# Kernel optimization log

Measured on AMD Instinct MI355X. Metric: run time of the kernel, lower is better.

Reference implementation:

```python
import jax, jax.numpy as jnp
import numpy as np

B, S, HID = 1, 2048, 4096
NH, NKV, HD = 32, 8, 128
WINDOW = 1024
ROPE_THETA = 1e6
NEG = -1e9


def rotate_half(x):
    x1, x2 = jnp.split(x, 2, axis=-1)
    return jnp.concatenate((-x2, x1), axis=-1)


def setup_inputs() -> dict:
    key = jax.random.key(0)
    ks = jax.random.split(key, 10)
    hidden_states = jax.random.normal(ks[0], (B, S, HID), jnp.float32)
    # rotary tables [max_pos, head_dim]
    inv_freq = 1.0 / (ROPE_THETA ** (jnp.arange(0, HD, 2, dtype=jnp.float32) / HD))
    t = jnp.arange(S, dtype=jnp.float32)
    freqs = jnp.outer(t, inv_freq)                       # [S, HD/2]
    emb = jnp.concatenate((freqs, freqs), axis=-1)       # [S, HD]
    cos, sin = jnp.cos(emb), jnp.sin(emb)
    position_ids = jnp.arange(S, dtype=jnp.int64)[None, :].astype(jnp.int32)
    # sliding-window causal additive mask [B,1,S,S]
    i = jnp.arange(S)[:, None]
    j = jnp.arange(S)[None, :]
    allowed = (j <= i) & (j > i - WINDOW)
    attention_mask = jnp.where(allowed, 0.0, NEG).astype(jnp.float32)[None, None]
    sc = 0.02
    Wq = jax.random.normal(ks[1], (HID, NH * HD), jnp.float32) * sc
    bq = jax.random.normal(ks[2], (NH * HD,), jnp.float32) * sc
    Wk = jax.random.normal(ks[3], (HID, NKV * HD), jnp.float32) * sc
    bk = jax.random.normal(ks[4], (NKV * HD,), jnp.float32) * sc
    Wv = jax.random.normal(ks[5], (HID, NKV * HD), jnp.float32) * sc
    bv = jax.random.normal(ks[6], (NKV * HD,), jnp.float32) * sc
    Wo = jax.random.normal(ks[7], (NH * HD, HID), jnp.float32) * sc
    bo = jax.random.normal(ks[8], (HID,), jnp.float32) * sc
    return dict(hidden_states=hidden_states, attention_mask=attention_mask,
                position_ids=position_ids, cos=cos, sin=sin,
                Wq=Wq, bq=bq, Wk=Wk, bk=bk, Wv=Wv, bv=bv, Wo=Wo, bo=bo)


def reference(hidden_states, attention_mask, position_ids, cos, sin,
              Wq, bq, Wk, bk, Wv, bv, Wo, bo):
    bsz, q_len, _ = hidden_states.shape
    q = (hidden_states @ Wq + bq).reshape(bsz, q_len, NH, HD).transpose(0, 2, 1, 3)
    k = (hidden_states @ Wk + bk).reshape(bsz, q_len, NKV, HD).transpose(0, 2, 1, 3)
    v = (hidden_states @ Wv + bv).reshape(bsz, q_len, NKV, HD).transpose(0, 2, 1, 3)
    # RoPE: cos/sin gathered by position_ids -> [B,1,S,HD]
    c = cos[position_ids][:, None]
    s = sin[position_ids][:, None]
    q = q * c + rotate_half(q) * s
    k = k * c + rotate_half(k) * s
    # GQA repeat_kv: [B,NKV,S,HD] -> [B,NH,S,HD]
    n_rep = NH // NKV
    k = jnp.repeat(k, n_rep, axis=1)
    v = jnp.repeat(v, n_rep, axis=1)
    scores = jnp.einsum('bhqd,bhkd->bhqk', q, k) / np.sqrt(HD).astype(np.float32)
    scores = scores + attention_mask[:, :, :, :k.shape[2]]
    probs = jax.nn.softmax(scores.astype(jnp.float32), axis=-1).astype(q.dtype)
    attn = jnp.einsum('bhqk,bhkd->bhqd', probs, v)
    attn = attn.transpose(0, 2, 1, 3).reshape(bsz, q_len, NH * HD)
    return attn @ Wo + bo
```

## Files before the change

kernel.cpp:

```cpp
#include <hip/hip_runtime.h>
#include <stdint.h>

typedef unsigned short u16;
typedef __attribute__((ext_vector_type(4))) float f32x4;
typedef __attribute__((ext_vector_type(16))) float f32x16;
typedef __attribute__((ext_vector_type(8))) __bf16 bf16x8;
typedef __attribute__((ext_vector_type(4))) u16 u16x4;
typedef __attribute__((ext_vector_type(8))) u16 u16x8;
typedef __attribute__((ext_vector_type(4))) unsigned int u32x4;

#define S_LEN 2048
#define HIDDEN 4096
#define NHEAD 32
#define NKVH 8
#define HD 128
#define WIN 1024

__device__ __forceinline__ float bf2f(u16 u) {
  union { unsigned int i; float f; } x; x.i = ((unsigned int)u) << 16; return x.f;
}
__device__ __forceinline__ u16 f2bf(float f) {
  union { float f; unsigned int i; } x; x.f = f;
  unsigned int r = x.i + 0x7FFFu + ((x.i >> 16) & 1u);
  return (u16)(r >> 16);
}

__device__ __forceinline__ void gload16(const void* g, void* l) {
  __builtin_amdgcn_global_load_lds((const __attribute__((address_space(1))) void*)g,
                                   (__attribute__((address_space(3))) void*)l, 16, 0, 0);
}

__device__ __forceinline__ unsigned int cvtpk_bf16(float a, float b) {
  unsigned int w;
  asm("v_cvt_pk_bf16_f32 %0, %1, %2" : "=v"(w) : "v"(a), "v"(b));
  return w;
}

__global__ __launch_bounds__(256) void conv_bf16_k(const float* __restrict__ in, u16* __restrict__ out) {
  size_t i = ((size_t)blockIdx.x * 256 + threadIdx.x) * 8;
  f32x4 a = *(const f32x4*)(in + i);
  f32x4 b = *(const f32x4*)(in + i + 4);
  u16x8 o;
  o[0] = f2bf(a[0]); o[1] = f2bf(a[1]); o[2] = f2bf(a[2]); o[3] = f2bf(a[3]);
  o[4] = f2bf(b[0]); o[5] = f2bf(b[1]); o[6] = f2bf(b[2]); o[7] = f2bf(b[3]);
  *(u16x8*)(out + i) = o;
}

__global__ __launch_bounds__(256) void concat_bias_k(const float* __restrict__ bq, const float* __restrict__ bk,
                                                     const float* __restrict__ bv, float* __restrict__ o) {
  int i = blockIdx.x * 256 + threadIdx.x;
  float v = (i < 4096) ? bq[i] : (i < 5120 ? bk[i - 4096] : bv[i - 5120]);
  o[i] = v;
}

template <typename TIN>
__global__ __launch_bounds__(256) void transpose_bf16_k(const TIN* __restrict__ in, int istride,
                                                        u16* __restrict__ out, int ostride) {
  __shared__ TIN tile[64][68];
  int r0 = blockIdx.x * 64, c0 = blockIdx.y * 64;
  int t = threadIdx.x;
  int tr = t >> 4;
  int tc = (t & 15) * 4;
#pragma unroll
  for (int i = 0; i < 4; ++i) {
    int r = i * 16 + tr;
    const TIN* src = in + (size_t)(r0 + r) * istride + c0 + tc;
    if constexpr (sizeof(TIN) == 4) {
      *(f32x4*)&tile[r][tc] = *(const f32x4*)src;
    } else {
      *(u16x4*)&tile[r][tc] = *(const u16x4*)src;
    }
  }
  __syncthreads();
#pragma unroll
  for (int i = 0; i < 4; ++i) {
    int rr = i * 16 + tr;
    u16x4 o;
#pragma unroll
    for (int j = 0; j < 4; ++j) {
      if constexpr (sizeof(TIN) == 4) o[j] = f2bf((float)tile[tc + j][rr]);
      else o[j] = (u16)tile[tc + j][rr];
    }
    *(u16x4*)(out + (size_t)(c0 + rr) * ostride + r0 + tc) = o;
  }
}

template <int BM, int BN, int MINW, typename TOUT>
__global__ __launch_bounds__(256, MINW) void gemm4_k(const u16* __restrict__ A, const u16* __restrict__ Bt,
                                                     const float* __restrict__ bias, TOUT* __restrict__ C,
                                                     int M, int N, int K) {
  constexpr int WM = BM / 2, WN = BN / 2;
  constexpr int MRA = WM / 16, MRB = WN / 16;
  constexpr int NA = BM / 64, NB = BN / 64;
  constexpr int NL = NA + NB;
  __shared__ __align__(16) u16 SA[3 * BM * 32];
  __shared__ __align__(16) u16 SB[3 * BN * 32];

  int tid = threadIdx.x;
  int w = tid >> 6, l = tid & 63;
  int cl = l & 15, g = l >> 4;
  int wr = w >> 1, wc = w & 1;

  int cpx = gridDim.x >> 3;
  int wg = (blockIdx.x & 7) * cpx + (blockIdx.x >> 3);
  int nbm = M / BM;
  int bm = wg % nbm, bn = wg / nbm;

  const u16* Ag = A + (size_t)(bm * BM) * K;
  const u16* Bg = Bt + (size_t)(bn * BN) * K;
  int srow = w * 16 + (l >> 2);
  int csrc = ((l & 3) ^ ((l >> 3) & 3)) * 8;
  int rdc = (g ^ ((cl >> 1) & 3)) << 3;

  f32x4 acc[MRA][MRB] = {};
  int NT = K >> 5;

  auto stage = [&](int slot, int tt, int h) {
    if (h < NA) {
      gload16(Ag + (size_t)(h * 64 + srow) * K + tt * 32 + csrc,
              (void*)(SA + slot * (BM * 32) + (h * 64 + w * 16) * 32));
    } else {
      int hb = h - NA;
      gload16(Bg + (size_t)(hb * 64 + srow) * K + tt * 32 + csrc,
              (void*)(SB + slot * (BN * 32) + (hb * 64 + w * 16) * 32));
    }
  };

#pragma unroll
  for (int h = 0; h < NL; ++h) stage(0, 0, h);
#pragma unroll
  for (int h = 0; h < NL; ++h) stage(1, 1, h);

  for (int t = 0; t < NT; ++t) {
    if constexpr (NL == 5) asm volatile("s_waitcnt vmcnt(5)" ::: "memory");
    else asm volatile("s_waitcnt vmcnt(4)" ::: "memory");
    __builtin_amdgcn_s_barrier();
    asm volatile("" ::: "memory");

    int slot = t % 3, ss = (t + 2) % 3;
    int ts = t + 2; if (ts >= NT) ts -= NT;
#pragma unroll
    for (int h = 0; h < NL; ++h) stage(ss, ts, h);

    const u16* sa = SA + slot * (BM * 32);
    const u16* sb = SB + slot * (BN * 32);
    bf16x8 af[MRA], bf[MRB];
#pragma unroll
    for (int mi = 0; mi < MRA; ++mi)
      af[mi] = *(const bf16x8*)(sa + (wr * WM + mi * 16 + cl) * 32 + rdc);
#pragma unroll
    for (int ni = 0; ni < MRB; ++ni)
      bf[ni] = *(const bf16x8*)(sb + (wc * WN + ni * 16 + cl) * 32 + rdc);
    __builtin_amdgcn_s_setprio(1);
#pragma unroll
    for (int mi = 0; mi < MRA; ++mi)
#pragma unroll
      for (int ni = 0; ni < MRB; ++ni)
        acc[mi][ni] = __builtin_amdgcn_mfma_f32_16x16x32_bf16(af[mi], bf[ni], acc[mi][ni], 0, 0, 0);
    __builtin_amdgcn_s_setprio(0);
  }

  asm volatile("s_waitcnt vmcnt(0)" ::: "memory");

#pragma unroll
  for (int mi = 0; mi < MRA; ++mi) {
    int row0 = bm * BM + wr * WM + mi * 16 + g * 4;
#pragma unroll
    for (int ni = 0; ni < MRB; ++ni) {
      int col = bn * BN + wc * WN + ni * 16 + cl;
      float bb = bias[col];
      f32x4 a = acc[mi][ni];
#pragma unroll
      for (int r = 0; r < 4; ++r) {
        float v = a[r] + bb;
        if constexpr (sizeof(TOUT) == 2) C[(size_t)(row0 + r) * N + col] = f2bf(v);
        else C[(size_t)(row0 + r) * N + col] = v;
      }
    }
  }
}

__global__ __launch_bounds__(256) void rope_scatter_k(const u16* __restrict__ qkv, const int* __restrict__ pos,
                                                      const float* __restrict__ cosT, const float* __restrict__ sinT,
                                                      u16* __restrict__ Q, u16* __restrict__ Kf) {
  int p = blockIdx.x * 256 + threadIdx.x;
  int s = p / 2560;
  int rem = p - s * 2560;
  int hs = rem >> 6;
  int d = rem & 63;
  int ps = pos[s];
  const float* cb = cosT + (size_t)ps * 128;
  const float* sb = sinT + (size_t)ps * 128;
  float c0 = cb[d], c1 = cb[d + 64], s0 = sb[d], s1 = sb[d + 64];
  if (hs < NHEAD) {
    const u16* src = qkv + (size_t)s * 6144 + hs * 128;
    float x0 = bf2f(src[d]), x1 = bf2f(src[d + 64]);
    const float qs = 0.08838834764831845f;
    u16* dst = Q + ((size_t)hs * S_LEN + s) * HD;
    dst[d] = f2bf((x0 * c0 - x1 * s0) * qs);
    dst[d + 64] = f2bf((x1 * c1 + x0 * s1) * qs);
  } else {
    int kh = hs - NHEAD;
    const u16* src = qkv + (size_t)s * 6144 + 4096 + kh * 128;
    float x0 = bf2f(src[d]), x1 = bf2f(src[d + 64]);
    int t = s >> 5, cr = s & 31;
    int ks = d >> 4, hi2 = (d >> 3) & 1, j = d & 7;
    size_t base = ((size_t)(kh * 64 + t) * 8 + ks) * 512 + (size_t)(cr + 32 * hi2) * 8 + j;
    Kf[base] = f2bf(x0 * c0 - x1 * s0);
    Kf[base + 4 * 512] = f2bf(x1 * c1 + x0 * s1);
  }
}

__global__ __launch_bounds__(256) void vfrag_k(const u16* __restrict__ qkv, u16* __restrict__ Vf) {
  __shared__ u16 tile[32][136];
  int bid = blockIdx.x;
  int kh = bid >> 6, t = bid & 63;
  int tid = threadIdx.x;
#pragma unroll
  for (int i = 0; i < 2; ++i) {
    int c = tid + i * 256;
    int r = c >> 4, seg = c & 15;
    *(u16x8*)&tile[r][seg * 8] =
        *(const u16x8*)(qkv + (size_t)(t * 32 + r) * 6144 + 5120 + kh * 128 + seg * 8);
  }
  __syncthreads();
#pragma unroll
  for (int i = 0; i < 2; ++i) {
    int pos = tid + i * 256;
    int dt = pos >> 7, sl = (pos >> 6) & 1, l = pos & 63;
    int c2 = l & 31, h2 = l >> 5;
    u16x8 o;
#pragma unroll
    for (int j = 0; j < 8; ++j) o[j] = tile[sl * 16 + h2 * 8 + j][dt * 32 + c2];
    *(u16x8*)(Vf + ((size_t)(kh * 512 + t * 8 + dt * 2 + sl)) * 512 + (size_t)l * 8) = o;
  }
}

__global__ __launch_bounds__(256, 2) void attn_k(const u16* __restrict__ Q, const u16* __restrict__ Kf,
                                                 const u16* __restrict__ Vf, u16* __restrict__ O) {
  int l = threadIdx.x & 63, w = threadIdx.x >> 6;
  int col = l & 31, hi = l >> 5;
  int bid = blockIdx.x;
  int kh = bid & 7;
  int head = (bid >> 3) & 3;
  int qbp = bid >> 5;
  int qb = (qbp & 1) ? (15 - (qbp >> 1)) : (qbp >> 1);
  int h = kh * 4 + head;
  int q0 = qb * 128 + w * 32;

  bf16x8 qf[8];
  const u16* qbase = Q + ((size_t)h * S_LEN + q0 + col) * HD + hi * 8;
#pragma unroll
  for (int ks = 0; ks < 8; ++ks) qf[ks] = *(const bf16x8*)(qbase + ks * 16);

  f32x16 ot[4];
#pragma unroll
  for (int dt = 0; dt < 4; ++dt)
#pragma unroll
    for (int r = 0; r < 16; ++r) ot[dt][r] = 0.f;
  float m_r = -3.0e38f, l_r = 0.f;

  const u16* kf0 = Kf + (size_t)kh * 64 * 4096 + (size_t)l * 8;
  const u16* vf0 = Vf + (size_t)kh * 512 * 512 + (size_t)l * 8;

  int jstart = q0 >= WIN ? q0 - WIN : 0;
  bf16x8 kfr[8];
  {
    const u16* kb = kf0 + (size_t)(jstart >> 5) * 4096;
#pragma unroll
    for (int ks = 0; ks < 8; ++ks) kfr[ks] = *(const bf16x8*)(kb + ks * 512);
  }

  for (int j0 = jstart; j0 <= q0; j0 += 32) {
    int t = j0 >> 5;
    f32x16 s = {};
#pragma unroll
    for (int ks = 0; ks < 8; ++ks)
      s = __builtin_amdgcn_mfma_f32_32x32x16_bf16(kfr[ks], qf[ks], s, 0, 0, 0);
    int tn = (j0 + 32 <= q0) ? (t + 1) : t;
    const u16* kbn = kf0 + (size_t)tn * 4096;
    bf16x8 kfn[8];
#pragma unroll
    for (int ks = 0; ks < 8; ++ks) kfn[ks] = *(const bf16x8*)(kbn + ks * 512);
    const u16* vb = vf0 + (size_t)t * 4096;
    bf16x8 vfr[8];
#pragma unroll
    for (int c = 0; c < 8; ++c) vfr[c] = *(const bf16x8*)(vb + c * 512);

    if (j0 + 31 > q0 || j0 < q0 - 992) {
      int q = q0 + col;
#pragma unroll
      for (int r = 0; r < 16; ++r) {
        int kv = j0 + (r & 3) + 8 * (r >> 2) + 4 * hi;
        if (kv > q || kv <= q - WIN) s[r] = -3.0e38f;
      }
    }
    float vm = fmaxf(fmaxf(fmaxf(s[0], s[1]), fmaxf(s[2], s[3])),
                     fmaxf(fmaxf(s[4], s[5]), fmaxf(s[6], s[7])));
    vm = fmaxf(vm, fmaxf(fmaxf(fmaxf(s[8], s[9]), fmaxf(s[10], s[11])),
                         fmaxf(fmaxf(s[12], s[13]), fmaxf(s[14], s[15]))));
    vm = fmaxf(vm, __shfl_xor(vm, 32));
    float mnew = fmaxf(m_r, vm);
    float sc = __expf(m_r - mnew);
    m_r = mnew;
    float rs = 0.f;
#pragma unroll
    for (int r = 0; r < 16; ++r) {
      float pv = __expf(s[r] - mnew);
      s[r] = pv;
      rs += pv;
    }
    rs += __shfl_xor(rs, 32);
    l_r = l_r * sc + rs;
#pragma unroll
    for (int dt = 0; dt < 4; ++dt)
#pragma unroll
      for (int r = 0; r < 16; ++r) ot[dt][r] *= sc;

    bf16x8 pb[2];
#pragma unroll
    for (int sl = 0; sl < 2; ++sl) {
      int b = sl * 8;
      unsigned int a0 = cvtpk_bf16(s[b + 0], s[b + 1]);
      unsigned int c0 = cvtpk_bf16(s[b + 4], s[b + 5]);
      asm("v_permlane32_swap_b32 %0, %1" : "+v"(a0), "+v"(c0));
      unsigned int a1 = cvtpk_bf16(s[b + 2], s[b + 3]);
      unsigned int c1 = cvtpk_bf16(s[b + 6], s[b + 7]);
      asm("v_permlane32_swap_b32 %0, %1" : "+v"(a1), "+v"(c1));
      u32x4 pv = {a0, a1, c0, c1};
      pb[sl] = __builtin_bit_cast(bf16x8, pv);
    }
#pragma unroll
    for (int dt = 0; dt < 4; ++dt) {
      ot[dt] = __builtin_amdgcn_mfma_f32_32x32x16_bf16(vfr[dt * 2 + 0], pb[0], ot[dt], 0, 0, 0);
      ot[dt] = __builtin_amdgcn_mfma_f32_32x32x16_bf16(vfr[dt * 2 + 1], pb[1], ot[dt], 0, 0, 0);
    }
#pragma unroll
    for (int ks = 0; ks < 8; ++ks) kfr[ks] = kfn[ks];
  }

  float inv = 1.0f / l_r;
#pragma unroll
  for (int dt = 0; dt < 4; ++dt) {
#pragma unroll
    for (int g2 = 0; g2 < 4; ++g2) {
      u16x4 o;
#pragma unroll
      for (int i = 0; i < 4; ++i) o[i] = f2bf(ot[dt][g2 * 4 + i] * inv);
      *(u16x4*)(O + (size_t)(q0 + col) * HIDDEN + h * HD + dt * 32 + g2 * 8 + hi * 4) = o;
    }
  }
}

extern "C" void kernel_launch(void* const* d_in, const int* in_sizes, int n_in,
                              void* d_out, int out_size, void* d_ws, size_t ws_size,
                              hipStream_t stream) {
  const float* X = (const float*)d_in[0];
  const int* pos = (const int*)d_in[2];
  const float* cosT = (const float*)d_in[3];
  const float* sinT = (const float*)d_in[4];
  const float* Wq = (const float*)d_in[5];
  const float* bq = (const float*)d_in[6];
  const float* Wk = (const float*)d_in[7];
  const float* bk = (const float*)d_in[8];
  const float* Wv = (const float*)d_in[9];
  const float* bv = (const float*)d_in[10];
  const float* Wo = (const float*)d_in[11];
  const float* bo = (const float*)d_in[12];
  float* out = (float*)d_out;

  const size_t MB = 1ull << 20;
  char* ws = (char*)d_ws;
  u16* WT = (u16*)ws;
  u16* Xb = (u16*)(ws + 48 * MB);
  u16* Qs = Xb;
  u16* QKVr = (u16*)(ws + 64 * MB);
  u16* attnO = QKVr;
  u16* Kfr = (u16*)(ws + 88 * MB);
  u16* Vfr = (u16*)(ws + 92 * MB);
  float* bqkv = (float*)(ws + 96 * MB);

  conv_bf16_k<<<4096, 256, 0, stream>>>(X, Xb);
  transpose_bf16_k<float><<<dim3(64, 64), 256, 0, stream>>>(Wq, 4096, WT, 4096);
  transpose_bf16_k<float><<<dim3(64, 16), 256, 0, stream>>>(Wk, 1024, WT + (size_t)4096 * 4096, 4096);
  transpose_bf16_k<float><<<dim3(64, 16), 256, 0, stream>>>(Wv, 1024, WT + (size_t)5120 * 4096, 4096);
  concat_bias_k<<<24, 256, 0, stream>>>(bq, bk, bv, bqkv);

  gemm4_k<128, 128, 3, u16><<<768, 256, 0, stream>>>(Xb, WT, bqkv, QKVr, 2048, 6144, 4096);

  rope_scatter_k<<<20480, 256, 0, stream>>>(QKVr, pos, cosT, sinT, Qs, Kfr);
  vfrag_k<<<512, 256, 0, stream>>>(QKVr, Vfr);
  transpose_bf16_k<float><<<dim3(64, 64), 256, 0, stream>>>(Wo, 4096, WT, 4096);

  attn_k<<<512, 256, 0, stream>>>(Qs, Kfr, Vfr, attnO);

  gemm4_k<128, 128, 3, float><<<512, 256, 0, stream>>>(attnO, WT, bo, out, 2048, 4096, 4096);
}
```

Measured before the change: 340.2 us.

## Replace 4-wave GEMM with 8-wave 256-wide tile GEMM with interleaved staging

Swaps the 256-thread 128x128 GEMM for a 512-thread kernel using 256-column (and 256- or 128-row) output tiles. Each iteration is split into phases that interleave global prefetch with MFMA work, separated by extra barriers. Larger tiles raise reuse of LDS data and cut global traffic per FLOP. The cost is fewer blocks (192/256) on a machine with many CUs, more registers per thread, and more barriers per K step.

```diff
diff --git a/kernel.cpp b/kernel.cpp
--- a/kernel.cpp
+++ b/kernel.cpp
@@ -85,21 +85,20 @@
   }
 }
 
-template <int BM, int BN, int MINW, typename TOUT>
-__global__ __launch_bounds__(256, MINW) void gemm4_k(const u16* __restrict__ A, const u16* __restrict__ Bt,
-                                                     const float* __restrict__ bias, TOUT* __restrict__ C,
-                                                     int M, int N, int K) {
-  constexpr int WM = BM / 2, WN = BN / 2;
-  constexpr int MRA = WM / 16, MRB = WN / 16;
-  constexpr int NA = BM / 64, NB = BN / 64;
-  constexpr int NL = NA + NB;
+template <int BM, typename TOUT>
+__global__ __launch_bounds__(512, 2) void gemm8_k(const u16* __restrict__ A, const u16* __restrict__ Bt,
+                                                  const float* __restrict__ bias, TOUT* __restrict__ C,
+                                                  int M, int N, int K) {
+  constexpr int MR = BM / 32;
+  constexpr int PH = MR / 2;
+  constexpr int NU = BM / 128 + 2;
   __shared__ __align__(16) u16 SA[3 * BM * 32];
-  __shared__ __align__(16) u16 SB[3 * BN * 32];
+  __shared__ __align__(16) u16 SB[3 * 256 * 32];
 
   int tid = threadIdx.x;
   int w = tid >> 6, l = tid & 63;
   int cl = l & 15, g = l >> 4;
-  int wr = w >> 1, wc = w & 1;
+  int wr = w >> 2, wc = w & 3;
 
   int cpx = gridDim.x >> 3;
   int wg = (blockIdx.x & 7) * cpx + (blockIdx.x >> 3);
@@ -107,67 +106,75 @@
   int bm = wg % nbm, bn = wg / nbm;
 
   const u16* Ag = A + (size_t)(bm * BM) * K;
-  const u16* Bg = Bt + (size_t)(bn * BN) * K;
-  int srow = w * 16 + (l >> 2);
-  int csrc = ((l & 3) ^ ((l >> 3) & 3)) * 8;
-  int rdc = (g ^ ((cl >> 1) & 3)) << 3;
-
-  f32x4 acc[MRA][MRB] = {};
+  const u16* Bg = Bt + (size_t)(bn * 256) * K;
+  int srow = tid >> 2;
+  int schunk = ((tid & 3) ^ ((tid >> 3) & 3)) * 8;
+  int rdc = (g ^ ((cl >> 1) & 3)) * 8;
+
+  f32x4 acc[MR][4] = {};
   int NT = K >> 5;
 
-  auto stage = [&](int slot, int tt, int h) {
-    if (h < NA) {
-      gload16(Ag + (size_t)(h * 64 + srow) * K + tt * 32 + csrc,
-              (void*)(SA + slot * (BM * 32) + (h * 64 + w * 16) * 32));
+  auto stage = [&](int slot, int tt, int u) {
+    if (u < BM / 128) {
+      gload16(Ag + (size_t)(u * 128 + srow) * K + tt * 32 + schunk,
+              (void*)(SA + slot * (BM * 32) + u * 4096 + tid * 8));
     } else {
-      int hb = h - NA;
-      gload16(Bg + (size_t)(hb * 64 + srow) * K + tt * 32 + csrc,
-              (void*)(SB + slot * (BN * 32) + (hb * 64 + w * 16) * 32));
+      int ub = u - BM / 128;
+      gload16(Bg + (size_t)(ub * 128 + srow) * K + tt * 32 + schunk,
+              (void*)(SB + slot * (256 * 32) + ub * 4096 + tid * 8));
     }
   };
 
 #pragma unroll
-  for (int h = 0; h < NL; ++h) stage(0, 0, h);
-#pragma unroll
-  for (int h = 0; h < NL; ++h) stage(1, 1, h);
+  for (int u = 0; u < NU; ++u) stage(0, 0, u);
+#pragma unroll
+  for (int u = 0; u < NU; ++u) stage(1, 1, u);
 
   for (int t = 0; t < NT; ++t) {
-    if constexpr (NL == 5) asm volatile("s_waitcnt vmcnt(5)" ::: "memory");
-    else asm volatile("s_waitcnt vmcnt(4)" ::: "memory");
+    if constexpr (NU == 4) asm volatile("s_waitcnt vmcnt(4)" ::: "memory");
+    else asm volatile("s_waitcnt vmcnt(3)" ::: "memory");
     __builtin_amdgcn_s_barrier();
     asm volatile("" ::: "memory");
 
     int slot = t % 3, ss = (t + 2) % 3;
     int ts = t + 2; if (ts >= NT) ts -= NT;
-#pragma unroll
-    for (int h = 0; h < NL; ++h) stage(ss, ts, h);
-
     const u16* sa = SA + slot * (BM * 32);
-    const u16* sb = SB + slot * (BN * 32);
-    bf16x8 af[MRA], bf[MRB];
-#pragma unroll
-    for (int mi = 0; mi < MRA; ++mi)
-      af[mi] = *(const bf16x8*)(sa + (wr * WM + mi * 16 + cl) * 32 + rdc);
-#pragma unroll
-    for (int ni = 0; ni < MRB; ++ni)
-      bf[ni] = *(const bf16x8*)(sb + (wc * WN + ni * 16 + cl) * 32 + rdc);
-    __builtin_amdgcn_s_setprio(1);
-#pragma unroll
-    for (int mi = 0; mi < MRA; ++mi)
-#pragma unroll
-      for (int ni = 0; ni < MRB; ++ni)
-        acc[mi][ni] = __builtin_amdgcn_mfma_f32_16x16x32_bf16(af[mi], bf[ni], acc[mi][ni], 0, 0, 0);
-    __builtin_amdgcn_s_setprio(0);
+    const u16* sb = SB + slot * (256 * 32);
+
+    bf16x8 bf[4];
+#pragma unroll
+    for (int p = 0; p < PH; ++p) {
+      bf16x8 a0 = *(const bf16x8*)(sa + (wr * (BM / 2) + (2 * p) * 16 + cl) * 32 + rdc);
+      bf16x8 a1 = *(const bf16x8*)(sa + (wr * (BM / 2) + (2 * p + 1) * 16 + cl) * 32 + rdc);
+      if (p == 0) {
+#pragma unroll
+        for (int ni = 0; ni < 4; ++ni)
+          bf[ni] = *(const bf16x8*)(sb + (wc * 64 + ni * 16 + cl) * 32 + rdc);
+      }
+#pragma unroll
+      for (int u = p * NU / PH; u < (p + 1) * NU / PH; ++u) stage(ss, ts, u);
+      __builtin_amdgcn_s_barrier();
+      asm volatile("s_waitcnt lgkmcnt(0)" ::: "memory");
+      __builtin_amdgcn_s_setprio(1);
+#pragma unroll
+      for (int ni = 0; ni < 4; ++ni) {
+        acc[2 * p][ni] = __builtin_amdgcn_mfma_f32_16x16x32_bf16(a0, bf[ni], acc[2 * p][ni], 0, 0, 0);
+        acc[2 * p + 1][ni] = __builtin_amdgcn_mfma_f32_16x16x32_bf16(a1, bf[ni], acc[2 * p + 1][ni], 0, 0, 0);
+      }
+      __builtin_amdgcn_s_setprio(0);
+      __builtin_amdgcn_s_barrier();
+      asm volatile("" ::: "memory");
+    }
   }
 
   asm volatile("s_waitcnt vmcnt(0)" ::: "memory");
 
 #pragma unroll
-  for (int mi = 0; mi < MRA; ++mi) {
-    int row0 = bm * BM + wr * WM + mi * 16 + g * 4;
-#pragma unroll
-    for (int ni = 0; ni < MRB; ++ni) {
-      int col = bn * BN + wc * WN + ni * 16 + cl;
+  for (int mi = 0; mi < MR; ++mi) {
+    int row0 = bm * BM + wr * (BM / 2) + mi * 16 + g * 4;
+#pragma unroll
+    for (int ni = 0; ni < 4; ++ni) {
+      int col = bn * 256 + wc * 64 + ni * 16 + cl;
       float bb = bias[col];
       f32x4 a = acc[mi][ni];
 #pragma unroll
@@ -386,7 +393,7 @@
   transpose_bf16_k<float><<<dim3(64, 16), 256, 0, stream>>>(Wv, 1024, WT + (size_t)5120 * 4096, 4096);
   concat_bias_k<<<24, 256, 0, stream>>>(bq, bk, bv, bqkv);
 
-  gemm4_k<128, 128, 3, u16><<<768, 256, 0, stream>>>(Xb, WT, bqkv, QKVr, 2048, 6144, 4096);
+  gemm8_k<256, u16><<<192, 512, 0, stream>>>(Xb, WT, bqkv, QKVr, 2048, 6144, 4096);
 
   rope_scatter_k<<<20480, 256, 0, stream>>>(QKVr, pos, cosT, sinT, Qs, Kfr);
   vfrag_k<<<512, 256, 0, stream>>>(QKVr, Vfr);
@@ -394,5 +401,5 @@
 
   attn_k<<<512, 256, 0, stream>>>(Qs, Kfr, Vfr, attnO);
 
-  gemm4_k<128, 128, 3, float><<<512, 256, 0, stream>>>(attnO, WT, bo, out, 2048, 4096, 4096);
-}
+  gemm8_k<128, float><<<256, 512, 0, stream>>>(attnO, WT, bo, out, 2048, 4096, 4096);
+}
```

Measured after the change: 413.0 us. 1.21x slower.
